# Kernel tuning notes

Measured on AMD Instinct MI355X. Metric: run time of the kernel, lower is better.

## Reference

```python
import jax, jax.numpy as jnp
import numpy as np

BT = 64  # chunk size (BLOCK_SIZE_C)
EPS = 1e-06


def setup_inputs() -> dict:
    key = jax.random.key(0)
    k1, k2, k3, k4 = jax.random.split(key, 4)
    B, H, S, D = 4, 8, 4096, 128
    q = jax.random.normal(k1, (B, H, S, D), dtype=jnp.float32)
    k = jax.random.normal(k2, (B, H, S, D), dtype=jnp.float32)
    v = jax.random.normal(k3, (B, H, S, D), dtype=jnp.float32)
    beta = jax.random.uniform(k4, (B, H, S), dtype=jnp.float32)
    return {"q": q, "k": k, "v": v, "beta": beta}


def _chunk_gated_delta_fwd(q, k, v, beta):
    # Recurrence: S_t = beta_t * S_{t-1} + k_t (x) v_t ;  o_t = q_t @ S_t
    B, H, S, D = q.shape
    NC = S // BT
    f32 = jnp.float32
    qf = q.astype(f32).reshape(B, H, NC, BT, D)
    kf = k.astype(f32).reshape(B, H, NC, BT, D)
    vf = v.astype(f32).reshape(B, H, NC, BT, D)
    log_beta = jnp.log(beta.astype(f32).reshape(B, H, NC, BT) + EPS)
    cum = jnp.cumsum(log_beta, axis=-1)                     # [B,H,NC,BT]
    tot = cum[..., -1]                                      # [B,H,NC]
    decay_from_start = jnp.exp(cum)                         # [B,H,NC,BT]
    decay_to_end = jnp.exp(tot[..., None] - cum)            # [B,H,NC,BT]
    causal = jnp.tril(jnp.ones((BT, BT), dtype=bool))
    decay_matrix = jnp.exp(cum[..., :, None] - cum[..., None, :])  # [B,H,NC,BT,BT]
    decay_masked = jnp.where(causal, decay_matrix, 0.0)
    # intra-chunk contribution (fully parallel across chunks)
    qk = jnp.einsum('bhcid,bhcjd->bhcij', qf, kf)
    out_intra = jnp.einsum('bhcij,bhcjd->bhcid', qk * decay_masked, vf)
    # per-chunk state-update term: (k * decay_to_end)^T @ v
    upd = jnp.einsum('bhcid,bhcie->bhcde', kf * decay_to_end[..., None], vf)
    # sequential inter-chunk recurrence over chunks
    def step(state, xs):
        qc, dfs_c, tot_c, upd_c = xs
        out_inter = jnp.einsum('bhid,bhde->bhie', qc * dfs_c[..., None], state)
        new_state = state * jnp.exp(tot_c)[..., None, None] + upd_c
        return new_state, out_inter
    xs = (jnp.moveaxis(qf, 2, 0), jnp.moveaxis(decay_from_start, 2, 0),
          jnp.moveaxis(tot, 2, 0), jnp.moveaxis(upd, 2, 0))
    state0 = jnp.zeros((B, H, D, D), dtype=f32)
    _, out_inter = jax.lax.scan(step, state0, xs)           # [NC,B,H,BT,D]
    out = out_intra + jnp.moveaxis(out_inter, 0, 2)
    return out.reshape(B, H, S, D).astype(q.dtype)


def reference(q, k, v, beta):
    return _chunk_gated_delta_fwd(q, k, v, beta)
```

## Files before the change

### kernel.cpp

```cpp
#include <hip/hip_runtime.h>
#include <math.h>

#define Gp  32
#define Sp  4096
#define Dp  128
#define BTp 64
#define NCp 64

typedef __attribute__((ext_vector_type(8))) short bf16x8;
typedef __attribute__((ext_vector_type(4))) float f32x4;

#define MFMA(a,b,c) __builtin_amdgcn_mfma_f32_16x16x32_bf16((a),(b),(c),0,0,0)

#define STR 72

__device__ inline unsigned short f2bf(float x) {
    union { float f; unsigned u; } u; u.f = x;
    unsigned r = u.u + 0x7fffu + ((u.u >> 16) & 1u);
    return (unsigned short)(r >> 16);
}
__device__ inline unsigned pack2(float lo, float hi) {
    return (unsigned)f2bf(lo) | ((unsigned)f2bf(hi) << 16);
}
__device__ inline float bflo(unsigned u) { union { unsigned u; float f; } t; t.u = u << 16; return t.f; }
__device__ inline float bfhi(unsigned u) { union { unsigned u; float f; } t; t.u = u & 0xffff0000u; return t.f; }

__global__ __launch_bounds__(256, 3) void gdn_intra(
    const float* __restrict__ q, const float* __restrict__ k,
    const float* __restrict__ v, const float* __restrict__ beta,
    float* __restrict__ out, unsigned short* __restrict__ upd,
    float* __restrict__ tot_buf, float* __restrict__ dfs_buf)
{
    __shared__ unsigned short s_k [64 * 128];
    __shared__ unsigned short s_vt[128 * STR];
    __shared__ unsigned short s_kt[128 * STR];

    const int blk = blockIdx.x, g = blk >> 6, c = blk & 63;
    const int tid = threadIdx.x, lane = tid & 63, w = tid >> 6;
    const int m16 = lane & 15, quad = lane >> 4;
    const size_t base  = ((size_t)g * Sp + (size_t)c * BTp) * Dp;
    const size_t bbase = (size_t)g * Sp + (size_t)c * BTp;

    float x = logf(beta[bbase + lane] + 1e-6f);
    #pragma unroll
    for (int off = 1; off < 64; off <<= 1) {
        float n = __shfl_up(x, off, 64);
        if (lane >= off) x += n;
    }
    const float tot = __shfl(x, 63, 64);
    const float dte_own = expf(tot - x);
    if (tid < 64) dfs_buf[bbase + lane] = expf(x);
    if (tid == 63) tot_buf[g * NCp + c] = tot;

    bf16x8 qf[4];
    {
        const float* qrow = q + base + (size_t)(16 * w + m16) * Dp + quad * 8;
        #pragma unroll
        for (int ks = 0; ks < 4; ++ks) {
            const float4 a = *(const float4*)(qrow + ks * 32);
            const float4 b = *(const float4*)(qrow + ks * 32 + 4);
            union { bf16x8 v; unsigned ui[4]; } t;
            t.ui[0] = pack2(a.x, a.y); t.ui[1] = pack2(a.z, a.w);
            t.ui[2] = pack2(b.x, b.y); t.ui[3] = pack2(b.z, b.w);
            qf[ks] = t.v;
        }
    }

    #pragma unroll 4
    for (int it = 0; it < 16; ++it) {
        const int p = it * 256 + tid;
        const int i = p >> 6, d = (p & 63) * 2;
        const float2 kv = *(const float2*)(k + base + (size_t)i * Dp + d);
        const int ad = i * 128 + ((((d >> 3) ^ (i & 15))) << 3) + (d & 7);
        *(unsigned*)&s_k[ad] = pack2(kv.x, kv.y);
    }
    #pragma unroll 4
    for (int it = 0; it < 16; ++it) {
        const int u = it * 256 + tid;
        const int d = u & 127, i = (u >> 7) * 2;
        const float dte0 = __shfl(dte_own, i, 64);
        const float dte1 = __shfl(dte_own, i + 1, 64);
        const float v0 = v[base + (size_t)i * Dp + d];
        const float v1 = v[base + (size_t)(i + 1) * Dp + d];
        const float k0 = k[base + (size_t)i * Dp + d] * dte0;
        const float k1 = k[base + (size_t)(i + 1) * Dp + d] * dte1;
        *(unsigned*)&s_vt[d * STR + i] = pack2(v0, v1);
        *(unsigned*)&s_kt[d * STR + i] = pack2(k0, k1);
    }
    __syncthreads();

    float pv[4][4];
    {
        f32x4 accP[4] = {};
        #pragma unroll
        for (int ks = 0; ks < 4; ++ks) {
            #pragma unroll
            for (int nt = 0; nt < 4; ++nt) {
                const int j = 16 * nt + m16;
                const bf16x8 bf = *(const bf16x8*)&s_k[j * 128 + (((quad + 4 * ks) ^ m16) << 3)];
                accP[nt] = MFMA(qf[ks], bf, accP[nt]);
            }
        }
        const int i0 = 16 * w + quad * 4;
        float cj[4];
        #pragma unroll
        for (int nt = 0; nt < 4; ++nt) cj[nt] = __shfl(x, 16 * nt + m16, 64);
        #pragma unroll
        for (int r = 0; r < 4; ++r) {
            const float ci = __shfl(x, i0 + r, 64);
            #pragma unroll
            for (int nt = 0; nt < 4; ++nt) {
                const int j = 16 * nt + m16;
                pv[nt][r] = (i0 + r >= j) ? accP[nt][r] * expf(ci - cj[nt]) : 0.f;
            }
        }
    }

    {
        f32x4 accU[2][8] = {};
        #pragma unroll
        for (int ks = 0; ks < 2; ++ks) {
            const bf16x8 a0 = *(const bf16x8*)&s_vt[(32 * w      + m16) * STR + quad * 8 + ks * 32];
            const bf16x8 a1 = *(const bf16x8*)&s_vt[(32 * w + 16 + m16) * STR + quad * 8 + ks * 32];
            #pragma unroll
            for (int nt = 0; nt < 8; ++nt) {
                const bf16x8 bf = *(const bf16x8*)&s_kt[(16 * nt + m16) * STR + quad * 8 + ks * 32];
                accU[0][nt] = MFMA(a0, bf, accU[0][nt]);
                accU[1][nt] = MFMA(a1, bf, accU[1][nt]);
            }
        }
        unsigned short* ub = upd + (size_t)blk * Dp * Dp;
        #pragma unroll
        for (int mt = 0; mt < 2; ++mt) {
            const int e0 = 32 * w + 16 * mt + quad * 4;
            #pragma unroll
            for (int nt = 0; nt < 8; ++nt) {
                const int d = 16 * nt + m16;
                #pragma unroll
                for (int r = 0; r < 4; ++r)
                    ub[(size_t)(e0 + r) * Dp + d] = f2bf(accU[mt][nt][r]);
            }
        }
    }
    __syncthreads();

    unsigned short* s_P = s_k;
    {
        const int i0 = 16 * w + quad * 4;
        #pragma unroll
        for (int r = 0; r < 4; ++r)
            #pragma unroll
            for (int nt = 0; nt < 4; ++nt)
                s_P[(i0 + r) * STR + 16 * nt + m16] = f2bf(pv[nt][r]);
    }
    __syncthreads();

    {
        f32x4 accO[8] = {};
        #pragma unroll
        for (int ks = 0; ks < 2; ++ks) {
            const bf16x8 af = *(const bf16x8*)&s_P[(16 * w + m16) * STR + quad * 8 + ks * 32];
            #pragma unroll
            for (int nt = 0; nt < 8; ++nt) {
                const bf16x8 bf = *(const bf16x8*)&s_vt[(16 * nt + m16) * STR + quad * 8 + ks * 32];
                accO[nt] = MFMA(af, bf, accO[nt]);
            }
        }
        const int i0 = 16 * w + quad * 4;
        #pragma unroll
        for (int nt = 0; nt < 8; ++nt) {
            const int d = 16 * nt + m16;
            #pragma unroll
            for (int r = 0; r < 4; ++r)
                out[base + (size_t)(i0 + r) * Dp + d] = accO[nt][r];
        }
    }
}

__global__ __launch_bounds__(256) void gdn_scan(
    unsigned short* __restrict__ upd, const float* __restrict__ tot_buf)
{
    const int g = blockIdx.x >> 4, slab = blockIdx.x & 15, tid = threadIdx.x;
    __shared__ float s_e[NCp];
    if (tid < NCp) s_e[tid] = expf(tot_buf[g * NCp + tid]);
    __syncthreads();
    unsigned* b = (unsigned*)upd + (size_t)g * NCp * 8192 + slab * 512 + tid;
    float st0 = 0.f, st1 = 0.f, st2 = 0.f, st3 = 0.f;
    unsigned u0a = b[0],    u1a = b[256];
    unsigned u0b = b[8192], u1b = b[8192 + 256];
    for (int cc = 0; cc < NCp; ++cc) {
        unsigned n0 = 0, n1 = 0;
        if (cc < NCp - 2) {
            n0 = b[(size_t)(cc + 2) * 8192];
            n1 = b[(size_t)(cc + 2) * 8192 + 256];
        }
        const float e = s_e[cc];
        b[(size_t)cc * 8192]       = pack2(st0, st1);
        b[(size_t)cc * 8192 + 256] = pack2(st2, st3);
        st0 = st0 * e + bflo(u0a);
        st1 = st1 * e + bfhi(u0a);
        st2 = st2 * e + bflo(u1a);
        st3 = st3 * e + bfhi(u1a);
        u0a = u0b; u1a = u1b; u0b = n0; u1b = n1;
    }
}

__global__ __launch_bounds__(256) void gdn_inter(
    const float* __restrict__ q, const unsigned short* __restrict__ state,
    const float* __restrict__ dfs_buf, float* __restrict__ out)
{
    const int blk = blockIdx.x, g = blk >> 6, c = blk & 63;
    const int tid = threadIdx.x, lane = tid & 63, w = tid >> 6;
    const int m16 = lane & 15, quad = lane >> 4;
    const size_t base  = ((size_t)g * Sp + (size_t)c * BTp) * Dp;
    const size_t bbase = (size_t)g * Sp + (size_t)c * BTp;
    const unsigned short* sb = state + (size_t)blk * Dp * Dp;

    const float scale = dfs_buf[bbase + 16 * w + m16];
    bf16x8 qf[4];
    const float* qrow = q + base + (size_t)(16 * w + m16) * Dp + quad * 8;
    #pragma unroll
    for (int ks = 0; ks < 4; ++ks) {
        const float4 a = *(const float4*)(qrow + ks * 32);
        const float4 b = *(const float4*)(qrow + ks * 32 + 4);
        union { bf16x8 v; unsigned ui[4]; } t;
        t.ui[0] = pack2(a.x * scale, a.y * scale);
        t.ui[1] = pack2(a.z * scale, a.w * scale);
        t.ui[2] = pack2(b.x * scale, b.y * scale);
        t.ui[3] = pack2(b.z * scale, b.w * scale);
        qf[ks] = t.v;
    }

    f32x4 acc[8] = {};
    #pragma unroll
    for (int ks = 0; ks < 4; ++ks) {
        #pragma unroll
        for (int nt = 0; nt < 8; ++nt) {
            const bf16x8 bf = *(const bf16x8*)(sb + (16 * nt + m16) * Dp + quad * 8 + ks * 32);
            acc[nt] = MFMA(qf[ks], bf, acc[nt]);
        }
    }
    const int i0 = 16 * w + quad * 4;
    #pragma unroll
    for (int nt = 0; nt < 8; ++nt) {
        const int e = 16 * nt + m16;
        #pragma unroll
        for (int r = 0; r < 4; ++r)
            out[base + (size_t)(i0 + r) * Dp + e] += acc[nt][r];
    }
}

extern "C" void kernel_launch(void* const* d_in, const int* in_sizes, int n_in,
                              void* d_out, int out_size, void* d_ws, size_t ws_size,
                              hipStream_t stream) {
    const float* q    = (const float*)d_in[0];
    const float* k    = (const float*)d_in[1];
    const float* v    = (const float*)d_in[2];
    const float* beta = (const float*)d_in[3];
    float* out = (float*)d_out;

    unsigned short* upd = (unsigned short*)d_ws;
    float* tot_buf = (float*)(upd + (size_t)Gp * NCp * Dp * Dp);
    float* dfs_buf = tot_buf + Gp * NCp;

    gdn_intra<<<Gp * NCp, 256, 0, stream>>>(q, k, v, beta, out, upd, tot_buf, dfs_buf);
    gdn_scan <<<Gp * 16, 256, 0, stream>>>(upd, tot_buf);
    gdn_inter<<<Gp * NCp, 256, 0, stream>>>(q, upd, dfs_buf, out);
}
```

Measured before the change: 326.6 us.

## Vectorize global loads in intra and scan kernels, prefetch out in inter

Converts the k/v staging loops in the intra kernel to float4/float2 loads, and replaces the manual bf16 packing with the HIP intrinsic conversion. The scan kernel now has 128 threads, each handling uint4 (8 bf16) with a 4-deep prefetch ring and a fully unrolled chunk loop. The inter kernel loads the existing output early and batches state fragment loads before the MFMAs, so memory latency can overlap compute. These changes aim to cut the number of memory instructions and hide latency, at the cost of more registers.

```diff
diff --git a/kernel.cpp b/kernel.cpp
--- a/kernel.cpp
+++ b/kernel.cpp
@@ -1,4 +1,5 @@
 #include <hip/hip_runtime.h>
+#include <hip/hip_bf16.h>
 #include <math.h>
 
 #define Gp  32
@@ -14,13 +15,14 @@
 
 #define STR 72
 
+__device__ inline unsigned pack2(float lo, float hi) {
+    __hip_bfloat162 h = __float22bfloat162_rn(make_float2(lo, hi));
+    union { __hip_bfloat162 v; unsigned u; } t; t.v = h; return t.u;
+}
 __device__ inline unsigned short f2bf(float x) {
     union { float f; unsigned u; } u; u.f = x;
     unsigned r = u.u + 0x7fffu + ((u.u >> 16) & 1u);
     return (unsigned short)(r >> 16);
-}
-__device__ inline unsigned pack2(float lo, float hi) {
-    return (unsigned)f2bf(lo) | ((unsigned)f2bf(hi) << 16);
 }
 __device__ inline float bflo(unsigned u) { union { unsigned u; float f; } t; t.u = u << 16; return t.f; }
 __device__ inline float bfhi(unsigned u) { union { unsigned u; float f; } t; t.u = u & 0xffff0000u; return t.f; }
@@ -66,26 +68,29 @@
         }
     }
 
-    #pragma unroll 4
-    for (int it = 0; it < 16; ++it) {
-        const int p = it * 256 + tid;
-        const int i = p >> 6, d = (p & 63) * 2;
-        const float2 kv = *(const float2*)(k + base + (size_t)i * Dp + d);
-        const int ad = i * 128 + ((((d >> 3) ^ (i & 15))) << 3) + (d & 7);
-        *(unsigned*)&s_k[ad] = pack2(kv.x, kv.y);
-    }
-    #pragma unroll 4
-    for (int it = 0; it < 16; ++it) {
+    #pragma unroll
+    for (int it = 0; it < 8; ++it) {
+        const int idx = (it * 256 + tid) * 4;
+        const int i = idx >> 7, d = idx & 127;
+        const float4 kv = *(const float4*)(k + base + (size_t)i * Dp + d);
+        const int ad = i * 128 + (((d >> 3) ^ (i & 15)) << 3) + (d & 7);
+        uint2 pw; pw.x = pack2(kv.x, kv.y); pw.y = pack2(kv.z, kv.w);
+        *(uint2*)&s_k[ad] = pw;
+    }
+    #pragma unroll
+    for (int it = 0; it < 8; ++it) {
         const int u = it * 256 + tid;
-        const int d = u & 127, i = (u >> 7) * 2;
+        const int d = (u & 63) * 2, i = (u >> 6) * 2;
         const float dte0 = __shfl(dte_own, i, 64);
         const float dte1 = __shfl(dte_own, i + 1, 64);
-        const float v0 = v[base + (size_t)i * Dp + d];
-        const float v1 = v[base + (size_t)(i + 1) * Dp + d];
-        const float k0 = k[base + (size_t)i * Dp + d] * dte0;
-        const float k1 = k[base + (size_t)(i + 1) * Dp + d] * dte1;
-        *(unsigned*)&s_vt[d * STR + i] = pack2(v0, v1);
-        *(unsigned*)&s_kt[d * STR + i] = pack2(k0, k1);
+        const float2 va = *(const float2*)(v + base + (size_t)i * Dp + d);
+        const float2 vb = *(const float2*)(v + base + (size_t)(i + 1) * Dp + d);
+        const float2 ka = *(const float2*)(k + base + (size_t)i * Dp + d);
+        const float2 kb = *(const float2*)(k + base + (size_t)(i + 1) * Dp + d);
+        *(unsigned*)&s_vt[d * STR + i]       = pack2(va.x, vb.x);
+        *(unsigned*)&s_vt[(d + 1) * STR + i] = pack2(va.y, vb.y);
+        *(unsigned*)&s_kt[d * STR + i]       = pack2(ka.x * dte0, kb.x * dte1);
+        *(unsigned*)&s_kt[(d + 1) * STR + i] = pack2(ka.y * dte0, kb.y * dte1);
     }
     __syncthreads();
 
@@ -177,31 +182,32 @@
     }
 }
 
-__global__ __launch_bounds__(256) void gdn_scan(
+__global__ __launch_bounds__(128) void gdn_scan(
     unsigned short* __restrict__ upd, const float* __restrict__ tot_buf)
 {
     const int g = blockIdx.x >> 4, slab = blockIdx.x & 15, tid = threadIdx.x;
     __shared__ float s_e[NCp];
     if (tid < NCp) s_e[tid] = expf(tot_buf[g * NCp + tid]);
     __syncthreads();
-    unsigned* b = (unsigned*)upd + (size_t)g * NCp * 8192 + slab * 512 + tid;
-    float st0 = 0.f, st1 = 0.f, st2 = 0.f, st3 = 0.f;
-    unsigned u0a = b[0],    u1a = b[256];
-    unsigned u0b = b[8192], u1b = b[8192 + 256];
+    uint4* b = (uint4*)(upd + (size_t)g * NCp * Dp * Dp) + slab * 128 + tid;
+    float s0 = 0.f, s1 = 0.f, s2 = 0.f, s3 = 0.f;
+    float s4 = 0.f, s5 = 0.f, s6 = 0.f, s7 = 0.f;
+    uint4 pf[4];
+    #pragma unroll
+    for (int j = 0; j < 4; ++j) pf[j] = b[(size_t)j * 2048];
+    #pragma unroll
     for (int cc = 0; cc < NCp; ++cc) {
-        unsigned n0 = 0, n1 = 0;
-        if (cc < NCp - 2) {
-            n0 = b[(size_t)(cc + 2) * 8192];
-            n1 = b[(size_t)(cc + 2) * 8192 + 256];
-        }
+        const uint4 cur = pf[cc & 3];
+        if (cc + 4 < NCp) pf[cc & 3] = b[(size_t)(cc + 4) * 2048];
         const float e = s_e[cc];
-        b[(size_t)cc * 8192]       = pack2(st0, st1);
-        b[(size_t)cc * 8192 + 256] = pack2(st2, st3);
-        st0 = st0 * e + bflo(u0a);
-        st1 = st1 * e + bfhi(u0a);
-        st2 = st2 * e + bflo(u1a);
-        st3 = st3 * e + bfhi(u1a);
-        u0a = u0b; u1a = u1b; u0b = n0; u1b = n1;
+        uint4 stq;
+        stq.x = pack2(s0, s1); stq.y = pack2(s2, s3);
+        stq.z = pack2(s4, s5); stq.w = pack2(s6, s7);
+        b[(size_t)cc * 2048] = stq;
+        s0 = s0 * e + bflo(cur.x); s1 = s1 * e + bfhi(cur.x);
+        s2 = s2 * e + bflo(cur.y); s3 = s3 * e + bfhi(cur.y);
+        s4 = s4 * e + bflo(cur.z); s5 = s5 * e + bfhi(cur.z);
+        s6 = s6 * e + bflo(cur.w); s7 = s7 * e + bfhi(cur.w);
     }
 }
 
@@ -215,6 +221,7 @@
     const size_t base  = ((size_t)g * Sp + (size_t)c * BTp) * Dp;
     const size_t bbase = (size_t)g * Sp + (size_t)c * BTp;
     const unsigned short* sb = state + (size_t)blk * Dp * Dp;
+    const int i0 = 16 * w + quad * 4;
 
     const float scale = dfs_buf[bbase + 16 * w + m16];
     bf16x8 qf[4];
@@ -231,22 +238,30 @@
         qf[ks] = t.v;
     }
 
+    float ov[8][4];
+    #pragma unroll
+    for (int nt = 0; nt < 8; ++nt)
+        #pragma unroll
+        for (int r = 0; r < 4; ++r)
+            ov[nt][r] = out[base + (size_t)(i0 + r) * Dp + 16 * nt + m16];
+
     f32x4 acc[8] = {};
     #pragma unroll
     for (int ks = 0; ks < 4; ++ks) {
-        #pragma unroll
-        for (int nt = 0; nt < 8; ++nt) {
-            const bf16x8 bf = *(const bf16x8*)(sb + (16 * nt + m16) * Dp + quad * 8 + ks * 32);
-            acc[nt] = MFMA(qf[ks], bf, acc[nt]);
-        }
-    }
-    const int i0 = 16 * w + quad * 4;
+        bf16x8 bfr[8];
+        #pragma unroll
+        for (int nt = 0; nt < 8; ++nt)
+            bfr[nt] = *(const bf16x8*)(sb + (16 * nt + m16) * Dp + quad * 8 + ks * 32);
+        #pragma unroll
+        for (int nt = 0; nt < 8; ++nt)
+            acc[nt] = MFMA(qf[ks], bfr[nt], acc[nt]);
+    }
     #pragma unroll
     for (int nt = 0; nt < 8; ++nt) {
         const int e = 16 * nt + m16;
         #pragma unroll
         for (int r = 0; r < 4; ++r)
-            out[base + (size_t)(i0 + r) * Dp + e] += acc[nt][r];
+            out[base + (size_t)(i0 + r) * Dp + e] = ov[nt][r] + acc[nt][r];
     }
 }
 
@@ -264,6 +279,6 @@
     float* dfs_buf = tot_buf + Gp * NCp;
 
     gdn_intra<<<Gp * NCp, 256, 0, stream>>>(q, k, v, beta, out, upd, tot_buf, dfs_buf);
-    gdn_scan <<<Gp * 16, 256, 0, stream>>>(upd, tot_buf);
+    gdn_scan <<<Gp * 16, 128, 0, stream>>>(upd, tot_buf);
     gdn_inter<<<Gp * NCp, 256, 0, stream>>>(q, upd, dfs_buf, out);
 }
```

Measured after the change: 314.8 us. 1.04x faster.
